# Kernel tuning notes

Hardware: AMD Instinct MI355X
Metric: run time of the kernel (lower is better)

Reference implementation:

```python
import jax, jax.numpy as jnp
import numpy as np

B, D, M, R, C = 4096, 16, 4, 2048, 10
EPS = 1e-9


def setup_inputs() -> dict:
    key = jax.random.key(0)
    k1, k2, k3, k4, k5 = jax.random.split(key, 5)
    x = jax.random.normal(k1, (B, D), dtype=jnp.float32)
    centers = jax.random.normal(k2, (D, M), dtype=jnp.float32)
    widths = jax.random.uniform(k3, (D, M), dtype=jnp.float32, minval=0.5, maxval=1.5)
    consequents = jax.random.uniform(k4, (R, D + 1, C), dtype=jnp.float32)
    rules = jax.random.randint(k5, (R, D), 0, M, dtype=jnp.int32)
    return {"x": x, "centers": centers, "widths": widths,
            "consequents": consequents, "rules": rules}


def reference(x, centers, widths, consequents, rules):
    batch = x.shape[0]
    # Gaussian membership values: (B, D, M)
    mfs = jnp.exp(-((x[:, :, None] - centers[None]) ** 2) / (2.0 * widths[None] ** 2))
    # Gather per-rule memberships: rule_mfs[b, d, r] = mfs[b, d, rules[r, d]] -> (B, D, R)
    idx = jnp.broadcast_to(rules.T[None].astype(jnp.int32), (batch, rules.shape[1], rules.shape[0]))
    rule_mfs = jnp.take_along_axis(mfs, idx, axis=2)
    # Firing strengths: product over input dims -> (B, R)
    fs = jnp.prod(rule_mfs, axis=1)
    norm_fs = fs / (jnp.sum(fs, axis=1, keepdims=True) + EPS)
    # Extended input with bias column -> (B, D+1)
    x_ext = jnp.concatenate([x, jnp.ones((batch, 1), dtype=x.dtype)], axis=1)
    # Faithful to torch.einsum('bi,rjc->brc', ...): i and j are both summed out
    rule_vals = jnp.einsum('bi,rjc->brc', x_ext, consequents)  # (B, R, C)
    out = jnp.einsum('br,brc->bc', norm_fs, rule_vals)  # (B, C)
    return out, norm_fs, x_ext
```

## Files before the change

### kernel.cpp

```cpp
#include <hip/hip_runtime.h>

#define BB 4096
#define DD 16
#define MM 4
#define RR 2048
#define CC 10
#define TB 4
#define RPT (RR / 256)

__global__ __launch_bounds__(256) void prep_kernel(
    const float* __restrict__ cons, const int* __restrict__ rules,
    float* __restrict__ wsumT, unsigned int* __restrict__ codes)
{
    int r = blockIdx.x * blockDim.x + threadIdx.x;
    if (r >= RR) return;
    const float* cr = cons + (size_t)r * (DD + 1) * CC;
    float s[CC];
#pragma unroll
    for (int c = 0; c < CC; ++c) s[c] = 0.0f;
#pragma unroll
    for (int j = 0; j < DD + 1; ++j) {
#pragma unroll
        for (int c = 0; c < CC; ++c) s[c] += cr[j * CC + c];
    }
#pragma unroll
    for (int c = 0; c < CC; ++c) wsumT[c * RR + r] = s[c];

    const int* rrp = rules + r * DD;
    unsigned int code = 0;
#pragma unroll
    for (int g = 0; g < 4; ++g) {
        unsigned int byte = 0;
#pragma unroll
        for (int k = 0; k < 4; ++k) byte |= (((unsigned int)rrp[g * 4 + k]) & 3u) << (2 * k);
        code |= byte << (8 * g);
    }
    codes[r] = code;
}

__global__ __launch_bounds__(256) void anfis_main(
    const float* __restrict__ x, const float* __restrict__ centers,
    const float* __restrict__ widths, const float* __restrict__ wsumT,
    const unsigned int* __restrict__ codes,
    float* __restrict__ out, float* __restrict__ norm_fs, float* __restrict__ x_ext)
{
    __shared__ __align__(16) char smraw[40 * 257 * 4];
    float* sb = (float*)smraw;
#define MF(row, dm)     sb[(row) * 64 + (dm)]
#define PAIRT(row, p, e) sb[256 + (row) * 128 + (p) * 16 + (e)]
#define QUADT(row, g, e) sb[768 + (row) * 1024 + (g) * 256 + (e)]
#define RED(v, t)       sb[(v) * 257 + (t)]

    __shared__ float xs[TB][DD];
    __shared__ float sx[TB];
    __shared__ float wpart[4][TB];
    __shared__ float invl[TB];
    __shared__ float oscale[TB];
    __shared__ float part2[40][4];

    const int tid = threadIdx.x;
    const int b0 = blockIdx.x * TB;

    if (tid < TB * DD) {
        int row = tid / DD, d = tid % DD;
        float v = x[(b0 + row) * DD + d];
        xs[row][d] = v;
        x_ext[(b0 + row) * (DD + 1) + d] = v;
    }
    if (tid < TB) x_ext[(b0 + tid) * (DD + 1) + DD] = 1.0f;
    __syncthreads();

    if (tid < TB) {
        float s = 1.0f;
#pragma unroll
        for (int d = 0; d < DD; ++d) s += xs[tid][d];
        sx[tid] = s;
    }

    {
        int row = tid >> 6, dm = tid & 63, d = dm >> 2, m = dm & 3;
        float c = centers[d * MM + m];
        float w = widths[d * MM + m];
        float z = xs[row][d] - c;
        MF(row, dm) = expf(-(z * z) / (2.0f * w * w));
    }
    __syncthreads();

#pragma unroll
    for (int i = tid; i < TB * 8 * 16; i += 256) {
        int row = i >> 7, rem = i & 127, p = rem >> 4, e = rem & 15;
        int i0 = e & 3, i1 = e >> 2;
        PAIRT(row, p, e) = MF(row, (2 * p) * 4 + i0) * MF(row, (2 * p + 1) * 4 + i1);
    }
    __syncthreads();

#pragma unroll
    for (int i = tid; i < TB * 4 * 256; i += 256) {
        int row = i >> 10, rem = i & 1023, g = rem >> 8, e = rem & 255;
        int lo = e & 15, hi = e >> 4;
        QUADT(row, g, e) = PAIRT(row, 2 * g, lo) * PAIRT(row, 2 * g + 1, hi);
    }
    __syncthreads();

    float fsreg[TB][RPT];
    float acc[TB][CC];
    float ssum[TB];
#pragma unroll
    for (int row = 0; row < TB; ++row) {
        ssum[row] = 0.0f;
#pragma unroll
        for (int c = 0; c < CC; ++c) acc[row][c] = 0.0f;
    }

#pragma unroll
    for (int j = 0; j < RPT; ++j) {
        int r = tid + 256 * j;
        unsigned int code = codes[r];
        float w[CC];
#pragma unroll
        for (int c = 0; c < CC; ++c) w[c] = wsumT[c * RR + r];
#pragma unroll
        for (int row = 0; row < TB; ++row) {
            float q0 = QUADT(row, 0, code & 255u);
            float q1 = QUADT(row, 1, (code >> 8) & 255u);
            float q2 = QUADT(row, 2, (code >> 16) & 255u);
            float q3 = QUADT(row, 3, code >> 24);
            float fs = (q0 * q1) * (q2 * q3);
            fsreg[row][j] = fs;
            ssum[row] += fs;
#pragma unroll
            for (int c = 0; c < CC; ++c) acc[row][c] = fmaf(fs, w[c], acc[row][c]);
        }
    }

    const int lane = tid & 63;
    const int wv = tid >> 6;
#pragma unroll
    for (int row = 0; row < TB; ++row) {
        float s = ssum[row];
#pragma unroll
        for (int off = 32; off > 0; off >>= 1) s += __shfl_xor(s, off, 64);
        if (lane == 0) wpart[wv][row] = s;
    }
    __syncthreads();
    if (tid < TB) {
        float t = wpart[0][tid] + wpart[1][tid] + wpart[2][tid] + wpart[3][tid];
        float inv = 1.0f / (t + 1e-9f);
        invl[tid] = inv;
        oscale[tid] = sx[tid] * inv;
    }
    __syncthreads();

#pragma unroll
    for (int row = 0; row < TB; ++row) {
        float inv = invl[row];
#pragma unroll
        for (int j = 0; j < RPT; ++j) {
            norm_fs[(size_t)(b0 + row) * RR + tid + 256 * j] = fsreg[row][j] * inv;
        }
    }

#pragma unroll
    for (int row = 0; row < TB; ++row) {
#pragma unroll
        for (int c = 0; c < CC; ++c) {
            RED(row * CC + c, tid) = acc[row][c];
        }
    }
    __syncthreads();
    if (tid < 160) {
        int v = tid % 40, ch = tid / 40;
        float s = 0.0f;
        int base = ch * 64;
        for (int i = 0; i < 64; ++i) s += RED(v, base + i);
        part2[v][ch] = s;
    }
    __syncthreads();
    if (tid < 40) {
        float val = part2[tid][0] + part2[tid][1] + part2[tid][2] + part2[tid][3];
        int row = tid / CC, c = tid % CC;
        out[(b0 + row) * CC + c] = oscale[row] * val;
    }
#undef MF
#undef PAIRT
#undef QUADT
#undef RED
}

extern "C" void kernel_launch(void* const* d_in, const int* in_sizes, int n_in,
                              void* d_out, int out_size, void* d_ws, size_t ws_size,
                              hipStream_t stream) {
    const float* x       = (const float*)d_in[0];
    const float* centers = (const float*)d_in[1];
    const float* widths  = (const float*)d_in[2];
    const float* cons    = (const float*)d_in[3];
    const int*   rules   = (const int*)d_in[4];

    float* out_p     = (float*)d_out;
    float* norm_fs_p = out_p + (size_t)BB * CC;
    float* x_ext_p   = norm_fs_p + (size_t)BB * RR;

    float* wsumT = (float*)d_ws;
    unsigned int* codes = (unsigned int*)((char*)d_ws + (size_t)CC * RR * sizeof(float));

    prep_kernel<<<(RR + 255) / 256, 256, 0, stream>>>(cons, rules, wsumT, codes);
    anfis_main<<<BB / TB, 256, 0, stream>>>(x, centers, widths, wsumT, codes,
                                            out_p, norm_fs_p, x_ext_p);
}
```

Before: 97.54 us.

## Interleave batch rows in float4 LUTs, partially reduce via shuffles, parallelize prep

The pair and quad membership tables now store all four batch rows as one float4 per entry. A single 128-bit LDS gather per quad index then replaces four scalar gathers, and the table build does about a quarter of the index work. The per-thread accumulator reduction first combines groups of four lanes with wave shuffles, which cuts the shared-memory reduction buffer and the serial sum loop by a factor of four. The prep kernel is split to one thread per (rule, class) pair so it uses more parallelism. Wider LDS gathers may raise bank conflicts, and the extra shuffles add some cost.

```diff
diff --git a/kernel.cpp b/kernel.cpp
--- a/kernel.cpp
+++ b/kernel.cpp
@@ -8,34 +8,34 @@
 #define TB 4
 #define RPT (RR / 256)
 
+typedef __attribute__((ext_vector_type(4))) float f32x4;
+
 __global__ __launch_bounds__(256) void prep_kernel(
     const float* __restrict__ cons, const int* __restrict__ rules,
     float* __restrict__ wsumT, unsigned int* __restrict__ codes)
 {
-    int r = blockIdx.x * blockDim.x + threadIdx.x;
-    if (r >= RR) return;
-    const float* cr = cons + (size_t)r * (DD + 1) * CC;
-    float s[CC];
-#pragma unroll
-    for (int c = 0; c < CC; ++c) s[c] = 0.0f;
-#pragma unroll
-    for (int j = 0; j < DD + 1; ++j) {
-#pragma unroll
-        for (int c = 0; c < CC; ++c) s[c] += cr[j * CC + c];
-    }
-#pragma unroll
-    for (int c = 0; c < CC; ++c) wsumT[c * RR + r] = s[c];
-
-    const int* rrp = rules + r * DD;
-    unsigned int code = 0;
-#pragma unroll
-    for (int g = 0; g < 4; ++g) {
-        unsigned int byte = 0;
-#pragma unroll
-        for (int k = 0; k < 4; ++k) byte |= (((unsigned int)rrp[g * 4 + k]) & 3u) << (2 * k);
-        code |= byte << (8 * g);
-    }
-    codes[r] = code;
+    int gid = blockIdx.x * 256 + threadIdx.x;
+    if (gid < RR * CC) {
+        int r = gid / CC, c = gid - r * CC;
+        const float* cr = cons + (size_t)r * (DD + 1) * CC + c;
+        float s = 0.0f;
+#pragma unroll
+        for (int j = 0; j < DD + 1; ++j) s += cr[j * CC];
+        wsumT[c * RR + r] = s;
+    }
+    if (gid < RR) {
+        const int* rrp = rules + gid * DD;
+        unsigned int code = 0;
+#pragma unroll
+        for (int g = 0; g < 4; ++g) {
+            unsigned int byt = 0;
+#pragma unroll
+            for (int k = 0; k < 4; ++k)
+                byt |= (((unsigned int)rrp[g * 4 + k]) & 3u) << (2 * k);
+            code |= byt << (8 * g);
+        }
+        codes[gid] = code;
+    }
 }
 
 __global__ __launch_bounds__(256) void anfis_main(
@@ -44,22 +44,21 @@
     const unsigned int* __restrict__ codes,
     float* __restrict__ out, float* __restrict__ norm_fs, float* __restrict__ x_ext)
 {
-    __shared__ __align__(16) char smraw[40 * 257 * 4];
-    float* sb = (float*)smraw;
-#define MF(row, dm)     sb[(row) * 64 + (dm)]
-#define PAIRT(row, p, e) sb[256 + (row) * 128 + (p) * 16 + (e)]
-#define QUADT(row, g, e) sb[768 + (row) * 1024 + (g) * 256 + (e)]
-#define RED(v, t)       sb[(v) * 257 + (t)]
-
+    __shared__ float MF[TB][64];
+    __shared__ f32x4 PAIR4[8][16];
+    __shared__ f32x4 QUAD4[4][256];
+    __shared__ float RED[TB * CC][68];
     __shared__ float xs[TB][DD];
     __shared__ float sx[TB];
     __shared__ float wpart[4][TB];
     __shared__ float invl[TB];
     __shared__ float oscale[TB];
-    __shared__ float part2[40][4];
+    __shared__ float part2[TB * CC][4];
 
     const int tid = threadIdx.x;
     const int b0 = blockIdx.x * TB;
+    const int lane = tid & 63;
+    const int wv = tid >> 6;
 
     if (tid < TB * DD) {
         int row = tid / DD, d = tid % DD;
@@ -82,23 +81,25 @@
         float c = centers[d * MM + m];
         float w = widths[d * MM + m];
         float z = xs[row][d] - c;
-        MF(row, dm) = expf(-(z * z) / (2.0f * w * w));
-    }
-    __syncthreads();
-
-#pragma unroll
-    for (int i = tid; i < TB * 8 * 16; i += 256) {
-        int row = i >> 7, rem = i & 127, p = rem >> 4, e = rem & 15;
+        MF[row][dm] = expf(-(z * z) / (2.0f * w * w));
+    }
+    __syncthreads();
+
+    if (tid < 8 * 16) {
+        int p = tid >> 4, e = tid & 15;
         int i0 = e & 3, i1 = e >> 2;
-        PAIRT(row, p, e) = MF(row, (2 * p) * 4 + i0) * MF(row, (2 * p + 1) * 4 + i1);
-    }
-    __syncthreads();
-
-#pragma unroll
-    for (int i = tid; i < TB * 4 * 256; i += 256) {
-        int row = i >> 10, rem = i & 1023, g = rem >> 8, e = rem & 255;
-        int lo = e & 15, hi = e >> 4;
-        QUADT(row, g, e) = PAIRT(row, 2 * g, lo) * PAIRT(row, 2 * g + 1, hi);
+        f32x4 v;
+#pragma unroll
+        for (int row = 0; row < TB; ++row)
+            v[row] = MF[row][(2 * p) * 4 + i0] * MF[row][(2 * p + 1) * 4 + i1];
+        PAIR4[p][e] = v;
+    }
+    __syncthreads();
+
+#pragma unroll
+    for (int i = tid; i < 4 * 256; i += 256) {
+        int g = i >> 8, e = i & 255;
+        QUAD4[g][e] = PAIR4[2 * g][e & 15] * PAIR4[2 * g + 1][e >> 4];
     }
     __syncthreads();
 
@@ -119,13 +120,13 @@
         float w[CC];
 #pragma unroll
         for (int c = 0; c < CC; ++c) w[c] = wsumT[c * RR + r];
+        f32x4 q0 = QUAD4[0][code & 255u];
+        f32x4 q1 = QUAD4[1][(code >> 8) & 255u];
+        f32x4 q2 = QUAD4[2][(code >> 16) & 255u];
+        f32x4 q3 = QUAD4[3][code >> 24];
 #pragma unroll
         for (int row = 0; row < TB; ++row) {
-            float q0 = QUADT(row, 0, code & 255u);
-            float q1 = QUADT(row, 1, (code >> 8) & 255u);
-            float q2 = QUADT(row, 2, (code >> 16) & 255u);
-            float q3 = QUADT(row, 3, code >> 24);
-            float fs = (q0 * q1) * (q2 * q3);
+            float fs = (q0[row] * q1[row]) * (q2[row] * q3[row]);
             fsreg[row][j] = fs;
             ssum[row] += fs;
 #pragma unroll
@@ -133,8 +134,6 @@
         }
     }
 
-    const int lane = tid & 63;
-    const int wv = tid >> 6;
 #pragma unroll
     for (int row = 0; row < TB; ++row) {
         float s = ssum[row];
@@ -164,27 +163,27 @@
     for (int row = 0; row < TB; ++row) {
 #pragma unroll
         for (int c = 0; c < CC; ++c) {
-            RED(row * CC + c, tid) = acc[row][c];
+            float s = acc[row][c];
+            s += __shfl_xor(s, 1, 64);
+            s += __shfl_xor(s, 2, 64);
+            if ((lane & 3) == 0) RED[row * CC + c][wv * 16 + (lane >> 2)] = s;
         }
     }
     __syncthreads();
     if (tid < 160) {
         int v = tid % 40, ch = tid / 40;
         float s = 0.0f;
-        int base = ch * 64;
-        for (int i = 0; i < 64; ++i) s += RED(v, base + i);
+        int base = ch * 16;
+#pragma unroll
+        for (int i = 0; i < 16; ++i) s += RED[v][base + i];
         part2[v][ch] = s;
     }
     __syncthreads();
-    if (tid < 40) {
+    if (tid < TB * CC) {
         float val = part2[tid][0] + part2[tid][1] + part2[tid][2] + part2[tid][3];
         int row = tid / CC, c = tid % CC;
         out[(b0 + row) * CC + c] = oscale[row] * val;
     }
-#undef MF
-#undef PAIRT
-#undef QUADT
-#undef RED
 }
 
 extern "C" void kernel_launch(void* const* d_in, const int* in_sizes, int n_in,
@@ -203,7 +202,7 @@
     float* wsumT = (float*)d_ws;
     unsigned int* codes = (unsigned int*)((char*)d_ws + (size_t)CC * RR * sizeof(float));
 
-    prep_kernel<<<(RR + 255) / 256, 256, 0, stream>>>(cons, rules, wsumT, codes);
+    prep_kernel<<<(RR * CC + 255) / 256, 256, 0, stream>>>(cons, rules, wsumT, codes);
     anfis_main<<<BB / TB, 256, 0, stream>>>(x, centers, widths, wsumT, codes,
                                             out_p, norm_fs_p, x_ext_p);
 }
```

Measured after the change: 91.00 us. 6.7% less time.
